# Optimization experiments

Hardware: AMD Instinct MI355X
Metric: run time of the kernel (lower is better)

The kernel has to match this reference:

```python
import jax, jax.numpy as jnp
import numpy as np

D_MODEL = 1024
N_HEAD = 16


def setup_inputs() -> dict:
    key = jax.random.key(0)
    ks = jax.random.split(key, 12)
    B, S, D = 4, 2048, D_MODEL
    scale = 1.0 / np.sqrt(D)
    inp = {
        "Q": jax.random.normal(ks[0], (B, S, D), jnp.float32),
        "K": jax.random.normal(ks[1], (B, S, D), jnp.float32),
        "V": jax.random.normal(ks[2], (B, S, D), jnp.float32),
        "Wq": jax.random.normal(ks[3], (D, D), jnp.float32) * scale,
        "bq": jax.random.normal(ks[4], (D,), jnp.float32) * scale,
        "Wk": jax.random.normal(ks[5], (D, D), jnp.float32) * scale,
        "bk": jax.random.normal(ks[6], (D,), jnp.float32) * scale,
        "Wv": jax.random.normal(ks[7], (D, D), jnp.float32) * scale,
        "bv": jax.random.normal(ks[8], (D,), jnp.float32) * scale,
        "Wo": jax.random.normal(ks[9], (D, D), jnp.float32) * scale,
        "bo": jax.random.normal(ks[10], (D,), jnp.float32) * scale,
    }
    return inp


def _split_heads(x, n_head):
    B, S, D = x.shape
    return x.reshape(B, S, n_head, D // n_head).transpose(0, 2, 1, 3)  # [B,H,S,dh]


def reference(Q, K, V, Wq, bq, Wk, bk, Wv, bv, Wo, bo):
    # torch Linear: x @ W.T + b
    q = _split_heads(Q @ Wq.T + bq, N_HEAD)
    k = _split_heads(K @ Wk.T + bk, N_HEAD)
    v = _split_heads(V @ Wv.T + bv, N_HEAD)
    d_k = k.shape[-1]
    score = jnp.einsum('bhqd,bhkd->bhqk', q, k) / jnp.sqrt(jnp.float32(d_k))
    attn = jax.nn.softmax(score, axis=-1)
    out = jnp.einsum('bhqk,bhkd->bhqd', attn, v)  # [B,H,S,dh]
    B, H, S, dh = out.shape
    out = out.transpose(0, 2, 1, 3).reshape(B, S, H * dh)
    return out @ Wo.T + bo
```

## Files before the change

### kernel.cpp

```cpp
#include <hip/hip_runtime.h>
#include <math.h>

#define D_MODEL 1024
#define N_HEAD  16
#define DH      64
#define SEQ     2048
#define BATCH   4
#define BH      (BATCH*N_HEAD)
#define MROWS   (BATCH*SEQ)

typedef __attribute__((ext_vector_type(8)))  short          s16x8;
typedef __attribute__((ext_vector_type(8)))  unsigned short u16x8;
typedef __attribute__((ext_vector_type(4)))  unsigned short u16x4;
typedef __attribute__((ext_vector_type(4)))  float          f32x4;
typedef __attribute__((ext_vector_type(16))) float          f32x16;
typedef __attribute__((ext_vector_type(4)))  unsigned int   u32x4;

#define QSCALE 0.18033688f

typedef const __attribute__((address_space(1))) unsigned int gu32;
typedef __attribute__((address_space(3))) unsigned int lu32;
#define GLOAD_LDS16(g, l) __builtin_amdgcn_global_load_lds((gu32*)(g), (lu32*)(l), 16, 0, 0)

__device__ __forceinline__ unsigned short f2bf(float x) {
    unsigned int u = __float_as_uint(x);
    u += 0x7FFFu + ((u >> 16) & 1u);
    return (unsigned short)(u >> 16);
}

__device__ __forceinline__ unsigned int cvtpk_bf16(float lo, float hi) {
    unsigned int r;
    asm("v_cvt_pk_bf16_f32 %0, %1, %2" : "=v"(r) : "v"(lo), "v"(hi));
    return r;
}

__device__ __forceinline__ float exp2_asm(float x) {
    float r;
    asm("v_exp_f32 %0, %1" : "=v"(r) : "v"(x));
    return r;
}

__device__ __forceinline__ float max3f(float a, float b, float c) {
    float r;
    asm("v_max3_f32 %0, %1, %2, %3" : "=v"(r) : "v"(a), "v"(b), "v"(c));
    return r;
}

__global__ __launch_bounds__(256) void conv_w4(const float* __restrict__ w0,
                                               const float* __restrict__ w1,
                                               const float* __restrict__ w2,
                                               const float* __restrict__ w3,
                                               unsigned short* __restrict__ o0,
                                               unsigned short* __restrict__ o1,
                                               unsigned short* __restrict__ o2,
                                               unsigned short* __restrict__ o3)
{
    const float* w; unsigned short* o;
    switch (blockIdx.y) {
        case 0:  w = w0; o = o0; break;
        case 1:  w = w1; o = o1; break;
        case 2:  w = w2; o = o2; break;
        default: w = w3; o = o3; break;
    }
    int i = blockIdx.x * 256 + threadIdx.x;
    const float4* p = (const float4*)w + (size_t)i * 2;
    float4 a = p[0], b = p[1];
    u16x8 v;
    v[0] = f2bf(a.x); v[1] = f2bf(a.y); v[2] = f2bf(a.z); v[3] = f2bf(a.w);
    v[4] = f2bf(b.x); v[5] = f2bf(b.y); v[6] = f2bf(b.z); v[7] = f2bf(b.w);
    *((u16x8*)o + i) = v;
}

template<int MODE, bool AF32>
__global__ __launch_bounds__(256) void gemm_bt(const void* __restrict__ Av,
                                               const unsigned short* __restrict__ W,
                                               const float* __restrict__ bias,
                                               unsigned short* __restrict__ outb,
                                               float* __restrict__ outf,
                                               float oscale)
{
    __shared__ short As[128 * 64];
    __shared__ short Bs[128 * 64];
    const int tid = threadIdx.x;
    const int w = tid >> 6, l = tid & 63;
    const int lr = l & 15, lg = l >> 4;
    const int wm = w >> 1, wn = w & 1;
    const int r0 = blockIdx.x * 128, c0 = blockIdx.y * 128;
    const int srow = tid >> 3;
    const int sc8  = tid & 7;

    f32x4 zz = {0.f, 0.f, 0.f, 0.f};
    f32x4 acc[4][4];
    #pragma unroll
    for (int i = 0; i < 4; ++i)
        #pragma unroll
        for (int j = 0; j < 4; ++j) acc[i][j] = zz;

    const unsigned short* Ab = (const unsigned short*)Av;
    const float*          Af = (const float*)Av;

    u16x8 ar[4], br[4];
    float4 arf[4][2];
    #pragma unroll
    for (int p = 0; p < 4; ++p) {
        int row = p * 32 + srow;
        if (AF32) {
            arf[p][0] = *(const float4*)(Af + (size_t)(r0 + row) * 1024 + sc8 * 8);
            arf[p][1] = *(const float4*)(Af + (size_t)(r0 + row) * 1024 + sc8 * 8 + 4);
        } else {
            ar[p] = *(const u16x8*)(Ab + (size_t)(r0 + row) * 1024 + sc8 * 8);
        }
        br[p] = *(const u16x8*)(W + (size_t)(c0 + row) * 1024 + sc8 * 8);
    }

    for (int ks = 0; ks < 16; ++ks) {
        __syncthreads();
        #pragma unroll
        for (int p = 0; p < 4; ++p) {
            int row = p * 32 + srow;
            if (AF32) {
                u32x4 wd;
                wd[0] = cvtpk_bf16(arf[p][0].x, arf[p][0].y);
                wd[1] = cvtpk_bf16(arf[p][0].z, arf[p][0].w);
                wd[2] = cvtpk_bf16(arf[p][1].x, arf[p][1].y);
                wd[3] = cvtpk_bf16(arf[p][1].z, arf[p][1].w);
                *(u16x8*)&As[row * 64 + ((sc8 ^ (row & 7)) * 8)] = __builtin_bit_cast(u16x8, wd);
            } else {
                *(u16x8*)&As[row * 64 + ((sc8 ^ (row & 7)) * 8)] = ar[p];
            }
            *(u16x8*)&Bs[row * 64 + ((sc8 ^ (row & 7)) * 8)] = br[p];
        }
        __syncthreads();
        if (ks < 15) {
            int k0 = (ks + 1) * 64;
            #pragma unroll
            for (int p = 0; p < 4; ++p) {
                int row = p * 32 + srow;
                if (AF32) {
                    arf[p][0] = *(const float4*)(Af + (size_t)(r0 + row) * 1024 + k0 + sc8 * 8);
                    arf[p][1] = *(const float4*)(Af + (size_t)(r0 + row) * 1024 + k0 + sc8 * 8 + 4);
                } else {
                    ar[p] = *(const u16x8*)(Ab + (size_t)(r0 + row) * 1024 + k0 + sc8 * 8);
                }
                br[p] = *(const u16x8*)(W + (size_t)(c0 + row) * 1024 + k0 + sc8 * 8);
            }
        }
        #pragma unroll
        for (int t = 0; t < 2; ++t) {
            const int k8 = lg + 4 * t;
            s16x8 af[4], bw[4];
            #pragma unroll
            for (int i = 0; i < 4; ++i) {
                int rowa = wm * 64 + i * 16 + lr;
                af[i] = *(const s16x8*)&As[rowa * 64 + ((k8 ^ (rowa & 7)) * 8)];
                int rowb = wn * 64 + i * 16 + lr;
                bw[i] = *(const s16x8*)&Bs[rowb * 64 + ((k8 ^ (rowb & 7)) * 8)];
            }
            #pragma unroll
            for (int i = 0; i < 4; ++i)
                #pragma unroll
                for (int j = 0; j < 4; ++j)
                    acc[i][j] = __builtin_amdgcn_mfma_f32_16x16x32_bf16(af[i], bw[j], acc[i][j], 0, 0, 0);
        }
    }

    #pragma unroll
    for (int i = 0; i < 4; ++i) {
        #pragma unroll
        for (int j = 0; j < 4; ++j) {
            const int colb = c0 + wn * 64 + j * 16 + lr;
            const float bv = bias[colb];
            if (MODE == 2) {
                const int row = r0 + wm * 64 + i * 16 + lg * 4;
                const int b = row >> 11, s = row & 2047;
                const int h = colb >> 6, d = colb & 63;
                u16x4 pv;
                pv[0] = f2bf((acc[i][j][0] + bv) * oscale);
                pv[1] = f2bf((acc[i][j][1] + bv) * oscale);
                pv[2] = f2bf((acc[i][j][2] + bv) * oscale);
                pv[3] = f2bf((acc[i][j][3] + bv) * oscale);
                *(u16x4*)(outb + ((size_t)(b * N_HEAD + h) * DH + d) * SEQ + s) = pv;
            } else {
                #pragma unroll
                for (int rg = 0; rg < 4; ++rg) {
                    const int row = r0 + wm * 64 + i * 16 + lg * 4 + rg;
                    const float v = acc[i][j][rg] + bv;
                    if (MODE == 0) {
                        outf[(size_t)row * D_MODEL + colb] = v;
                    } else {
                        const int b = row >> 11, s = row & 2047;
                        const int h = colb >> 6, d = colb & 63;
                        outb[((size_t)(b * N_HEAD + h) * SEQ + s) * DH + d] = f2bf(v * oscale);
                    }
                }
            }
        }
    }
}

__global__ __launch_bounds__(256, 4) void flash_attn_mfma32(const unsigned short* __restrict__ qb,
                                                            const unsigned short* __restrict__ kb,
                                                            const unsigned short* __restrict__ vtb,
                                                            unsigned short* __restrict__ aob)
{
    __shared__ u16x8 Kt[2][512];
    __shared__ u16x8 Vt[2][512];

    const int tid = threadIdx.x;
    const int w = tid >> 6, l = tid & 63;
    const int q32 = l & 31;
    const int h = l >> 5;

    const int wg   = blockIdx.x;
    const int xcd  = wg & 7;
    const int slot = wg >> 3;
    const int bh   = xcd * 8 + (slot >> 4);
    const int qt   = slot & 15;

    const unsigned short* qh = qb + (size_t)bh * SEQ * DH;
    const char* kptr = (const char*)(kb + (size_t)bh * SEQ * DH);
    const char* vptr = (const char*)(vtb + (size_t)bh * DH * SEQ);

    const int qrow = qt * 128 + w * 32 + q32;

    s16x8 qf[4];
    #pragma unroll
    for (int ks = 0; ks < 4; ++ks)
        qf[ks] = *(const s16x8*)(qh + (size_t)qrow * DH + ks * 16 + h * 8);

    f32x16 O[2], Ls;
    #pragma unroll
    for (int r = 0; r < 16; ++r) { O[0][r] = 0.f; O[1][r] = 0.f; Ls[r] = 0.f; }
    float m = 0.f;

    u16x8 onesv;
    #pragma unroll
    for (int r = 0; r < 8; ++r) onesv[r] = 0x3F80;
    const s16x8 ones = __builtin_bit_cast(s16x8, onesv);

    size_t koff[2], voff[2];
    #pragma unroll
    for (int p = 0; p < 2; ++p) {
        const int chunk = 2 * w + p;
        const int rowp = l ^ chunk;
        koff[p] = (size_t)rowp * (DH * 2) + chunk * 16;
        voff[p] = (size_t)rowp * (SEQ * 2) + chunk * 16;
    }

    #pragma unroll
    for (int p = 0; p < 2; ++p) {
        const int chunk = 2 * w + p;
        GLOAD_LDS16(kptr + koff[p], &Kt[0][chunk * 64]);
        GLOAD_LDS16(vptr + voff[p], &Vt[0][chunk * 64]);
    }
    __syncthreads();

    int buf = 0;
    for (int kv = 0; kv < SEQ / 64; ++kv) {
        if (kv < SEQ / 64 - 1) {
            #pragma unroll
            for (int p = 0; p < 2; ++p) {
                const int chunk = 2 * w + p;
                GLOAD_LDS16(kptr + (size_t)(kv + 1) * (64 * DH * 2) + koff[p], &Kt[buf ^ 1][chunk * 64]);
                GLOAD_LDS16(vptr + (size_t)(kv + 1) * 128 + voff[p], &Vt[buf ^ 1][chunk * 64]);
            }
        }

        f32x16 SC[2];
        #pragma unroll
        for (int r = 0; r < 16; ++r) { SC[0][r] = -m; SC[1][r] = -m; }
        __builtin_amdgcn_s_setprio(1);
        #pragma unroll
        for (int ks = 0; ks < 4; ++ks) {
            const int chunk = 2 * ks + h;
            #pragma unroll
            for (int c = 0; c < 2; ++c) {
                const int row = c * 32 + q32;
                s16x8 kf = __builtin_bit_cast(s16x8, Kt[buf][chunk * 64 + (row ^ chunk)]);
                SC[c] = __builtin_amdgcn_mfma_f32_32x32x16_bf16(kf, qf[ks], SC[c], 0, 0, 0);
            }
        }
        __builtin_amdgcn_s_setprio(0);

        #define GETSC(i) ((i) < 16 ? SC[0][(i)] : SC[1][(i) - 16])
        float t0[11];
        #pragma unroll
        for (int r = 0; r < 10; ++r)
            t0[r] = max3f(GETSC(3 * r), GETSC(3 * r + 1), GETSC(3 * r + 2));
        t0[10] = fmaxf(GETSC(30), GETSC(31));
        float u0 = max3f(t0[0], t0[1], t0[2]);
        float u1 = max3f(t0[3], t0[4], t0[5]);
        float u2 = max3f(t0[6], t0[7], t0[8]);
        float u3 = fmaxf(t0[9], t0[10]);
        float rmb_l = fmaxf(max3f(u0, u1, u2), u3);
        float rmb = fmaxf(rmb_l, __shfl_xor(rmb_l, 32, 64));
        #undef GETSC

        if (!__all(rmb <= 8.0f)) {
            const float delta = fmaxf(rmb, 0.f);
            const float fold = exp2_asm(-delta);
            Ls *= fold;
            O[0] *= fold;
            O[1] *= fold;
            m += delta;
            #pragma unroll
            for (int c = 0; c < 2; ++c)
                #pragma unroll
                for (int r = 0; r < 16; ++r)
                    SC[c][r] -= delta;
        }

        #pragma unroll
        for (int c = 0; c < 2; ++c)
            #pragma unroll
            for (int r = 0; r < 16; ++r)
                SC[c][r] = exp2_asm(SC[c][r]);

        s16x8 pa[4];
        #pragma unroll
        for (int s = 0; s < 4; ++s) {
            const int c = s >> 1, rb = (s & 1) * 8;
            unsigned int a0 = cvtpk_bf16(SC[c][rb + 0], SC[c][rb + 1]);
            unsigned int a1 = cvtpk_bf16(SC[c][rb + 2], SC[c][rb + 3]);
            unsigned int b0 = cvtpk_bf16(SC[c][rb + 4], SC[c][rb + 5]);
            unsigned int b1 = cvtpk_bf16(SC[c][rb + 6], SC[c][rb + 7]);
            unsigned int x0 = (unsigned int)__shfl_xor((int)a0, 32, 64);
            unsigned int x1 = (unsigned int)__shfl_xor((int)a1, 32, 64);
            unsigned int y0 = (unsigned int)__shfl_xor((int)b0, 32, 64);
            unsigned int y1 = (unsigned int)__shfl_xor((int)b1, 32, 64);
            u32x4 wd;
            wd[0] = h ? y0 : a0;
            wd[1] = h ? y1 : a1;
            wd[2] = h ? b0 : x0;
            wd[3] = h ? b1 : x1;
            pa[s] = __builtin_bit_cast(s16x8, wd);
        }

        __builtin_amdgcn_s_setprio(1);
        #pragma unroll
        for (int s = 0; s < 4; ++s) {
            const int chunk = 2 * s + h;
            #pragma unroll
            for (int c = 0; c < 2; ++c) {
                const int row = c * 32 + q32;
                s16x8 vf = __builtin_bit_cast(s16x8, Vt[buf][chunk * 64 + (row ^ chunk)]);
                O[c] = __builtin_amdgcn_mfma_f32_32x32x16_bf16(vf, pa[s], O[c], 0, 0, 0);
            }
            Ls = __builtin_amdgcn_mfma_f32_32x32x16_bf16(ones, pa[s], Ls, 0, 0, 0);
        }
        __builtin_amdgcn_s_setprio(0);

        if (kv < SEQ / 64 - 1) {
            __syncthreads();
            buf ^= 1;
        }
    }

    const float inv = 1.0f / Ls[0];
    const int b = bh >> 4, head = bh & 15;
    unsigned short* obase = aob + ((size_t)b * SEQ + qrow) * D_MODEL + head * DH;
    #pragma unroll
    for (int c = 0; c < 2; ++c) {
        #pragma unroll
        for (int rq = 0; rq < 4; ++rq) {
            const int d0 = 8 * rq + 4 * h + 32 * c;
            u16x4 pv;
            #pragma unroll
            for (int j = 0; j < 4; ++j) pv[j] = f2bf(O[c][rq * 4 + j] * inv);
            *(u16x4*)(obase + d0) = pv;
        }
    }
}

extern "C" void kernel_launch(void* const* d_in, const int* in_sizes, int n_in,
                              void* d_out, int out_size, void* d_ws, size_t ws_size,
                              hipStream_t stream)
{
    const float* Q  = (const float*)d_in[0];
    const float* K  = (const float*)d_in[1];
    const float* V  = (const float*)d_in[2];
    const float* Wq = (const float*)d_in[3];
    const float* bq = (const float*)d_in[4];
    const float* Wk = (const float*)d_in[5];
    const float* bk = (const float*)d_in[6];
    const float* Wv = (const float*)d_in[7];
    const float* bv = (const float*)d_in[8];
    const float* Wo = (const float*)d_in[9];
    const float* bo = (const float*)d_in[10];

    const size_t PER = (size_t)MROWS * D_MODEL;
    const size_t WSZ = (size_t)D_MODEL * D_MODEL;
    unsigned short* wqb = (unsigned short*)d_ws;
    unsigned short* wkb = wqb + WSZ;
    unsigned short* wvb = wkb + WSZ;
    unsigned short* wob = wvb + WSZ;
    unsigned short* qb2 = wob + WSZ;
    unsigned short* kb2 = qb2 + PER;
    unsigned short* vtb = kb2 + PER;
    unsigned short* aob = vtb + PER;

    dim3 gg(MROWS / 128, D_MODEL / 128);

    conv_w4<<<dim3(512, 4), 256, 0, stream>>>(Wq, Wk, Wv, Wo, wqb, wkb, wvb, wob);

    gemm_bt<1, true><<<gg, 256, 0, stream>>>(Q, wqb, bq, qb2, nullptr, QSCALE);
    gemm_bt<1, true><<<gg, 256, 0, stream>>>(K, wkb, bk, kb2, nullptr, 1.0f);
    gemm_bt<2, true><<<gg, 256, 0, stream>>>(V, wvb, bv, vtb, nullptr, 1.0f);

    flash_attn_mfma32<<<dim3(16 * BH), 256, 0, stream>>>(qb2, kb2, vtb, aob);

    gemm_bt<0, false><<<gg, 256, 0, stream>>>(aob, wob, bo, nullptr, (float*)d_out, 1.0f);
}
```

Before: 247.4 us.

## Swap GEMM B-tile to direct LDS loads, attention K/V to register staging, use permlane32 swap

In the projection GEMM, the weight tile is now loaded straight into shared memory with global_load_lds using an XOR-swizzled source address, instead of being staged through registers. In the attention kernel, the reverse happens: K and V tiles are loaded into registers and stored to shared memory after the PV step, replacing the earlier direct-to-LDS loads. The cross-half exchange of P fragments now uses v_permlane32_swap instead of four shuffles plus selects. Each change moves a transfer between the direct-to-LDS path and register staging, which trades register pressure against load latency hiding differently in each kernel.

```diff
diff --git a/kernel.cpp b/kernel.cpp
--- a/kernel.cpp
+++ b/kernel.cpp
@@ -99,7 +99,14 @@
     const unsigned short* Ab = (const unsigned short*)Av;
     const float*          Af = (const float*)Av;
 
-    u16x8 ar[4], br[4];
+    const int lrow8 = l >> 3;
+    const int lslot = l & 7;
+    size_t bsrc[4];
+    #pragma unroll
+    for (int p = 0; p < 4; ++p)
+        bsrc[p] = ((size_t)(c0 + w * 32 + p * 8 + lrow8) * 1024 + (size_t)((lslot ^ lrow8) * 8)) * 2;
+
+    u16x8 ar[4];
     float4 arf[4][2];
     #pragma unroll
     for (int p = 0; p < 4; ++p) {
@@ -110,11 +117,13 @@
         } else {
             ar[p] = *(const u16x8*)(Ab + (size_t)(r0 + row) * 1024 + sc8 * 8);
         }
-        br[p] = *(const u16x8*)(W + (size_t)(c0 + row) * 1024 + sc8 * 8);
     }
 
     for (int ks = 0; ks < 16; ++ks) {
         __syncthreads();
+        #pragma unroll
+        for (int p = 0; p < 4; ++p)
+            GLOAD_LDS16((const char*)W + bsrc[p] + (size_t)ks * 128, &Bs[(w * 32 + p * 8) * 64]);
         #pragma unroll
         for (int p = 0; p < 4; ++p) {
             int row = p * 32 + srow;
@@ -128,7 +137,6 @@
             } else {
                 *(u16x8*)&As[row * 64 + ((sc8 ^ (row & 7)) * 8)] = ar[p];
             }
-            *(u16x8*)&Bs[row * 64 + ((sc8 ^ (row & 7)) * 8)] = br[p];
         }
         __syncthreads();
         if (ks < 15) {
@@ -142,7 +150,6 @@
                 } else {
                     ar[p] = *(const u16x8*)(Ab + (size_t)(r0 + row) * 1024 + k0 + sc8 * 8);
                 }
-                br[p] = *(const u16x8*)(W + (size_t)(c0 + row) * 1024 + k0 + sc8 * 8);
             }
         }
         #pragma unroll
@@ -218,8 +225,8 @@
     const int qt   = slot & 15;
 
     const unsigned short* qh = qb + (size_t)bh * SEQ * DH;
-    const char* kptr = (const char*)(kb + (size_t)bh * SEQ * DH);
-    const char* vptr = (const char*)(vtb + (size_t)bh * DH * SEQ);
+    const unsigned short* kh = kb + (size_t)bh * SEQ * DH;
+    const unsigned short* vh = vtb + (size_t)bh * DH * SEQ;
 
     const int qrow = qt * 128 + w * 32 + q32;
 
@@ -238,31 +245,33 @@
     for (int r = 0; r < 8; ++r) onesv[r] = 0x3F80;
     const s16x8 ones = __builtin_bit_cast(s16x8, onesv);
 
-    size_t koff[2], voff[2];
+    const int srow = tid >> 3;
+    const int sc8  = tid & 7;
+
+    u16x8 kreg[2], vreg[2];
     #pragma unroll
     for (int p = 0; p < 2; ++p) {
-        const int chunk = 2 * w + p;
-        const int rowp = l ^ chunk;
-        koff[p] = (size_t)rowp * (DH * 2) + chunk * 16;
-        voff[p] = (size_t)rowp * (SEQ * 2) + chunk * 16;
-    }
-
+        int rr = p * 32 + srow;
+        kreg[p] = *(const u16x8*)(kh + (size_t)rr * DH + sc8 * 8);
+        vreg[p] = *(const u16x8*)(vh + (size_t)rr * SEQ + sc8 * 8);
+    }
     #pragma unroll
     for (int p = 0; p < 2; ++p) {
-        const int chunk = 2 * w + p;
-        GLOAD_LDS16(kptr + koff[p], &Kt[0][chunk * 64]);
-        GLOAD_LDS16(vptr + voff[p], &Vt[0][chunk * 64]);
+        int rr = p * 32 + srow;
+        Kt[0][sc8 * 64 + (rr ^ sc8)] = kreg[p];
+        Vt[0][sc8 * 64 + (rr ^ sc8)] = vreg[p];
     }
     __syncthreads();
 
     int buf = 0;
     for (int kv = 0; kv < SEQ / 64; ++kv) {
         if (kv < SEQ / 64 - 1) {
+            const int s0 = (kv + 1) * 64;
             #pragma unroll
             for (int p = 0; p < 2; ++p) {
-                const int chunk = 2 * w + p;
-                GLOAD_LDS16(kptr + (size_t)(kv + 1) * (64 * DH * 2) + koff[p], &Kt[buf ^ 1][chunk * 64]);
-                GLOAD_LDS16(vptr + (size_t)(kv + 1) * 128 + voff[p], &Vt[buf ^ 1][chunk * 64]);
+                int rr = p * 32 + srow;
+                kreg[p] = *(const u16x8*)(kh + (size_t)(s0 + rr) * DH + sc8 * 8);
+                vreg[p] = *(const u16x8*)(vh + (size_t)rr * SEQ + s0 + sc8 * 8);
             }
         }
 
@@ -324,15 +333,13 @@
             unsigned int a1 = cvtpk_bf16(SC[c][rb + 2], SC[c][rb + 3]);
             unsigned int b0 = cvtpk_bf16(SC[c][rb + 4], SC[c][rb + 5]);
             unsigned int b1 = cvtpk_bf16(SC[c][rb + 6], SC[c][rb + 7]);
-            unsigned int x0 = (unsigned int)__shfl_xor((int)a0, 32, 64);
-            unsigned int x1 = (unsigned int)__shfl_xor((int)a1, 32, 64);
-            unsigned int y0 = (unsigned int)__shfl_xor((int)b0, 32, 64);
-            unsigned int y1 = (unsigned int)__shfl_xor((int)b1, 32, 64);
+            asm volatile("v_permlane32_swap_b32 %0, %1" : "+v"(a0), "+v"(b0));
+            asm volatile("v_permlane32_swap_b32 %0, %1" : "+v"(a1), "+v"(b1));
             u32x4 wd;
-            wd[0] = h ? y0 : a0;
-            wd[1] = h ? y1 : a1;
-            wd[2] = h ? b0 : x0;
-            wd[3] = h ? b1 : x1;
+            wd[0] = a0;
+            wd[1] = a1;
+            wd[2] = b0;
+            wd[3] = b1;
             pa[s] = __builtin_bit_cast(s16x8, wd);
         }
 
@@ -351,6 +358,12 @@
         __builtin_amdgcn_s_setprio(0);
 
         if (kv < SEQ / 64 - 1) {
+            #pragma unroll
+            for (int p = 0; p < 2; ++p) {
+                int rr = p * 32 + srow;
+                Kt[buf ^ 1][sc8 * 64 + (rr ^ sc8)] = kreg[p];
+                Vt[buf ^ 1][sc8 * 64 + (rr ^ sc8)] = vreg[p];
+            }
             __syncthreads();
             buf ^= 1;
         }
```

Measured after the change: 237.1 us. 4.2% less time.
